# Optimization experiments

Measured on AMD Instinct MI355X. Metric: run time of the kernel, lower is better.

## Reference

```python
import jax, jax.numpy as jnp
import numpy as np

N, D, C = 2048, 192, 100000
S, M = 30.0, 0.2

def setup_inputs() -> dict:
    key = jax.random.key(0)
    k1, k2, k3 = jax.random.split(key, 3)
    x = jax.random.normal(k1, (N, D), dtype=jnp.float32)
    W = jax.random.normal(k2, (C, D), dtype=jnp.float32) * 0.05
    label = jax.random.randint(k3, (N,), 0, C, dtype=jnp.int64)
    return {"x": x, "W": W, "label": label}

def reference(x, W, label):
    # NOTE: the original torch code's weight-normalization loop is a no-op
    # (it rebinds the local name W, never mutating the parameter), so W is
    # intentionally NOT normalized here; only x is.
    xn = x / jnp.linalg.norm(x, axis=1, keepdims=True)          # [N, D]
    wf = jnp.einsum("nd,cd->nc", xn, W)                          # [N, C]
    tgt = jnp.take_along_axis(wf, label[:, None], axis=1)[:, 0]  # [N]
    numer = S * (tgt - M)                                        # margin-adjusted target logit
    logits = S * wf
    # replace the label column with the margin-adjusted numerator so that
    # logsumexp(logits) == log(exp(numer) + sum_{j!=y} exp(s*wf[:,j]))
    logits = logits.at[jnp.arange(N), label].set(numer)
    L = numer - jax.nn.logsumexp(logits, axis=1)                 # [N]
    return -jnp.mean(L)
```

## Files before the change

kernel.cpp:

```cpp
#include <hip/hip_runtime.h>
#include <stdint.h>


constexpr int N  = 2048;
constexpr int D  = 192;
constexpr int C  = 100000;
constexpr int KT = D / 32;
constexpr int TILE = 512;
constexpr int RT16 = C / 16;
constexpr int TPG = 12;
constexpr int CX = 523;
constexpr int NT16 = CX * TPG;
constexpr float PHANTOM = (float)(NT16 * 16 - C);
constexpr int BANDS = 4;
constexpr int RYB = N / (64 * BANDS);
constexpr int BUF = 4 * KT * TILE;
constexpr int NXB = N / 4;

#define S_SCALE 30.0f
#define MARGIN  0.2f
#define S_LOG2E 43.2808512266689f

using short8 = __attribute__((ext_vector_type(8))) short;
using f32x4  = __attribute__((ext_vector_type(4))) float;

typedef __attribute__((address_space(1))) const void GV;
typedef __attribute__((address_space(3))) void LV;

__device__ inline unsigned short f2bf(float f) {
  unsigned int u = __float_as_uint(f);
  u += 0x7fffu + ((u >> 16) & 1u);
  return (unsigned short)(u >> 16);
}

__device__ inline int pack_idx(int r, int k) {
  return ((r >> 4) * KT + (k >> 5)) * TILE + (((k >> 3) & 3) * 16 + (r & 15)) * 8 + (k & 7);
}

__device__ inline float row_sum16(float v) {
  int x;
  x = __float_as_int(v);
  v += __int_as_float(__builtin_amdgcn_update_dpp(0, x, 0x128, 0xF, 0xF, true));
  x = __float_as_int(v);
  v += __int_as_float(__builtin_amdgcn_update_dpp(0, x, 0x124, 0xF, 0xF, true));
  x = __float_as_int(v);
  v += __int_as_float(__builtin_amdgcn_update_dpp(0, x, 0x04E, 0xF, 0xF, true));
  x = __float_as_int(v);
  v += __int_as_float(__builtin_amdgcn_update_dpp(0, x, 0x0B1, 0xF, 0xF, true));
  return v;
}

__global__ __launch_bounds__(256) void prep_x(
    const float* __restrict__ x, unsigned short* __restrict__ xnb,
    float* __restrict__ out) {
  const int bid  = blockIdx.x;
  const int lane = threadIdx.x & 63;
  if (bid == 0 && threadIdx.x == 0) out[0] = 0.0f;

  const int row = bid * 4 + (threadIdx.x >> 6);
  const float* xr = x + (size_t)row * D;
  float v0 = xr[lane], v1 = xr[lane + 64], v2 = xr[lane + 128];
  float ss = v0 * v0 + v1 * v1 + v2 * v2;
#pragma unroll
  for (int off = 32; off > 0; off >>= 1) ss += __shfl_xor(ss, off, 64);
  const float inv = rsqrtf(ss) * S_LOG2E;
  xnb[pack_idx(row, lane)]       = f2bf(v0 * inv);
  xnb[pack_idx(row, lane + 64)]  = f2bf(v1 * inv);
  xnb[pack_idx(row, lane + 128)] = f2bf(v2 * inv);
}

__global__ __launch_bounds__(256, 3) void gemm_lse(
    const unsigned short* __restrict__ xnb,
    const float* __restrict__ W,
    float* __restrict__ partial) {
  __shared__ alignas(16) unsigned short As[2 * BUF];
  __shared__ alignas(16) float rs_lds[4][256];

  const int tid = threadIdx.x;
  const int bid = blockIdx.x;
  const int cx = bid >> 3, ry = bid & 7;

  {
    const unsigned short* slab = xnb + (size_t)(ry * BANDS) * BUF;
#pragma unroll
    for (int i = 0; i < 6; ++i) {
      const int chunk = tid + i * 256;
      __builtin_amdgcn_global_load_lds(
          (GV*)((const char*)slab + (size_t)chunk * 16),
          (LV*)((char*)As + (size_t)chunk * 16), 16, 0, 0);
    }
  }

  const int lane = tid & 63, wave = tid >> 6;
  const int m = lane & 15, quad = lane >> 4;

  short8 breg[3][KT];
#pragma unroll
  for (int tc = 0; tc < 3; ++tc) {
    const int t16 = cx * TPG + wave * 3 + tc;
    if (t16 < RT16) {
      const float* src = W + (size_t)(t16 * 16 + m) * D + quad * 8;
#pragma unroll
      for (int ks = 0; ks < KT; ++ks) {
        const float4* s4 = (const float4*)(src + ks * 32);
        float4 f0 = s4[0], f1 = s4[1];
        short8 hv;
        hv[0] = (short)f2bf(f0.x); hv[1] = (short)f2bf(f0.y);
        hv[2] = (short)f2bf(f0.z); hv[3] = (short)f2bf(f0.w);
        hv[4] = (short)f2bf(f1.x); hv[5] = (short)f2bf(f1.y);
        hv[6] = (short)f2bf(f1.z); hv[7] = (short)f2bf(f1.w);
        breg[tc][ks] = hv;
      }
    } else {
      const short8 z = {0, 0, 0, 0, 0, 0, 0, 0};
#pragma unroll
      for (int ks = 0; ks < KT; ++ks) breg[tc][ks] = z;
    }
  }

  const f32x4 zero4 = {0.0f, 0.0f, 0.0f, 0.0f};

  for (int b = 0; b < BANDS; ++b) {
    __syncthreads();

    if (b + 1 < BANDS) {
      const unsigned short* slab = xnb + (size_t)(ry * BANDS + b + 1) * BUF;
      char* dst = (char*)&As[((b + 1) & 1) * BUF];
#pragma unroll
      for (int i = 0; i < 6; ++i) {
        const int chunk = tid + i * 256;
        __builtin_amdgcn_global_load_lds(
            (GV*)((const char*)slab + (size_t)chunk * 16),
            (LV*)(dst + (size_t)chunk * 16), 16, 0, 0);
      }
    }

    const unsigned short* Ab = &As[(b & 1) * BUF];

    f32x4 acc[4][3];
#pragma unroll
    for (int a = 0; a < 4; ++a)
#pragma unroll
      for (int c = 0; c < 3; ++c) acc[a][c] = zero4;

#pragma unroll
    for (int ks = 0; ks < KT; ++ks) {
      short8 af[4];
#pragma unroll
      for (int tr = 0; tr < 4; ++tr)
        af[tr] = *(const short8*)(&Ab[(tr * KT + ks) * TILE + lane * 8]);
#pragma unroll
      for (int tr = 0; tr < 4; ++tr)
#pragma unroll
        for (int tc = 0; tc < 3; ++tc)
          acc[tr][tc] = __builtin_amdgcn_mfma_f32_16x16x32_bf16(
              af[tr], breg[tc][ks], acc[tr][tc], 0, 0, 0);
    }

#pragma unroll
    for (int tr = 0; tr < 4; ++tr) {
      float rv0 = 0.f, rv1 = 0.f, rv2 = 0.f, rv3 = 0.f;
#pragma unroll
      for (int tc = 0; tc < 3; ++tc) {
        rv0 += __builtin_amdgcn_exp2f(acc[tr][tc][0]);
        rv1 += __builtin_amdgcn_exp2f(acc[tr][tc][1]);
        rv2 += __builtin_amdgcn_exp2f(acc[tr][tc][2]);
        rv3 += __builtin_amdgcn_exp2f(acc[tr][tc][3]);
      }
      rv0 = row_sum16(rv0);
      rv1 = row_sum16(rv1);
      rv2 = row_sum16(rv2);
      rv3 = row_sum16(rv3);
      if (m == 0) {
        float4 v = make_float4(rv0, rv1, rv2, rv3);
        *(float4*)(&rs_lds[wave][b * 64 + tr * 16 + quad * 4]) = v;
      }
    }
  }

  __syncthreads();
  if (tid < 256) {
    const float s = rs_lds[0][tid] + rs_lds[1][tid] + rs_lds[2][tid] + rs_lds[3][tid];
    partial[(size_t)cx * N + ry * 256 + tid] = s;
  }
}

__global__ __launch_bounds__(256) void finalize_rows(
    const float* __restrict__ x, const float* __restrict__ W,
    const int* __restrict__ label, const float* __restrict__ partial,
    float* __restrict__ out) {
  const int row  = blockIdx.x * 4 + (threadIdx.x >> 6);
  const int lane = threadIdx.x & 63;
  const float* xr = x + (size_t)row * D;
  float v0 = xr[lane], v1 = xr[lane + 64], v2 = xr[lane + 128];
  float ss = v0 * v0 + v1 * v1 + v2 * v2;
  const int lab = label[row];
  const float* wr = W + (size_t)lab * D;
  float d = v0 * wr[lane] + v1 * wr[lane + 64] + v2 * wr[lane + 128];
  float p = 0.0f;
  for (int s = lane; s < CX; s += 64) p += partial[(size_t)s * N + row];
#pragma unroll
  for (int off = 32; off > 0; off >>= 1) {
    ss += __shfl_xor(ss, off, 64);
    d  += __shfl_xor(d,  off, 64);
    p  += __shfl_xor(p,  off, 64);
  }
  __shared__ float part[4];
  if (lane == 0) {
    const float tgt   = d * rsqrtf(ss);
    const float numer = S_SCALE * (tgt - MARGIN);
    const float se = p - PHANTOM - __expf(S_SCALE * tgt) + __expf(numer);
    part[threadIdx.x >> 6] = numer - logf(se);
  }
  __syncthreads();
  if (threadIdx.x == 0) {
    const float blocksum = part[0] + part[1] + part[2] + part[3];
    atomicAdd(out, -blocksum * (1.0f / (float)N));
  }
}

extern "C" void kernel_launch(void* const* d_in, const int* in_sizes, int n_in,
                              void* d_out, int out_size, void* d_ws, size_t ws_size,
                              hipStream_t stream) {
  const float* x     = (const float*)d_in[0];
  const float* W     = (const float*)d_in[1];
  const int*   label = (const int*)d_in[2];
  float*       out   = (float*)d_out;

  char* ws = (char*)d_ws;
  size_t off = 0;
  unsigned short* xnb = (unsigned short*)(ws + off); off += (size_t)N * D * 2;
  float* partial = (float*)(ws + off); off += (size_t)CX * N * 4;

  prep_x<<<NXB, 256, 0, stream>>>(x, xnb, out);

  gemm_lse<<<CX * RYB, 256, 0, stream>>>(xnb, W, partial);

  finalize_rows<<<N / 4, 256, 0, stream>>>(x, W, label, partial, out);
}
```

Measured before the change: 216.2 us.

## Make gemm_lse persistent with XCD-aware work assignment and cross-tile x prefetch

Replaces the one-block-per-tile grid with a persistent grid of 768 blocks. Each block loops over (column tile, row quarter) work items, with column tiles assigned per XCD, and doubles the bands per item so each converted W register tile is reused across more rows. It prefetches the first x band of the next work item during the last band, streams per-band row sums out with double-buffered LDS instead of a single end-of-item write, and converts W to bf16 with the packed v_cvt_pk_bf16_f32 instruction. The aim is to cut launch and tail overhead and to lower W reload and conversion cost, in exchange for more complex loop control and fewer resident blocks.

```diff
diff --git a/kernel.cpp b/kernel.cpp
--- a/kernel.cpp
+++ b/kernel.cpp
@@ -12,10 +12,14 @@
 constexpr int CX = 523;
 constexpr int NT16 = CX * TPG;
 constexpr float PHANTOM = (float)(NT16 * 16 - C);
-constexpr int BANDS = 4;
+constexpr int BANDS = 8;
 constexpr int RYB = N / (64 * BANDS);
 constexpr int BUF = 4 * KT * TILE;
 constexpr int NXB = N / 4;
+constexpr int CXG = 66;
+constexpr int JMAX = CXG * RYB;
+constexpr int SLOTS = 96;
+constexpr int GRID = SLOTS * 8;
 
 #define S_SCALE 30.0f
 #define MARGIN  0.2f
@@ -31,6 +35,12 @@
   unsigned int u = __float_as_uint(f);
   u += 0x7fffu + ((u >> 16) & 1u);
   return (unsigned short)(u >> 16);
+}
+
+__device__ inline unsigned int cvtpk(float lo, float hi) {
+  unsigned int r;
+  asm("v_cvt_pk_bf16_f32 %0, %1, %2" : "=v"(r) : "v"(lo), "v"(hi));
+  return r;
 }
 
 __device__ inline int pack_idx(int r, int k) {
@@ -69,119 +79,131 @@
   xnb[pack_idx(row, lane + 128)] = f2bf(v2 * inv);
 }
 
+#define DMA_BAND(DSTBYTES, SLABIDX)                                          \
+  {                                                                          \
+    const char* _src = (const char*)(xnb + (size_t)(SLABIDX) * BUF);         \
+    char* _dst = (char*)As + (size_t)(DSTBYTES);                             \
+    _Pragma("unroll")                                                        \
+    for (int _i = 0; _i < 6; ++_i) {                                         \
+      const int _c = tid + _i * 256;                                         \
+      __builtin_amdgcn_global_load_lds((GV*)(_src + (size_t)_c * 16),        \
+                                       (LV*)(_dst + (size_t)_c * 16), 16, 0, 0); \
+    }                                                                        \
+  }
+
 __global__ __launch_bounds__(256, 3) void gemm_lse(
     const unsigned short* __restrict__ xnb,
     const float* __restrict__ W,
     float* __restrict__ partial) {
   __shared__ alignas(16) unsigned short As[2 * BUF];
-  __shared__ alignas(16) float rs_lds[4][256];
+  __shared__ alignas(16) float rs[2][4][64];
 
   const int tid = threadIdx.x;
   const int bid = blockIdx.x;
-  const int cx = bid >> 3, ry = bid & 7;
-
-  {
-    const unsigned short* slab = xnb + (size_t)(ry * BANDS) * BUF;
-#pragma unroll
-    for (int i = 0; i < 6; ++i) {
-      const int chunk = tid + i * 256;
-      __builtin_amdgcn_global_load_lds(
-          (GV*)((const char*)slab + (size_t)chunk * 16),
-          (LV*)((char*)As + (size_t)chunk * 16), 16, 0, 0);
-    }
-  }
-
+  const int xcd = bid & 7, slot = bid >> 3;
   const int lane = tid & 63, wave = tid >> 6;
   const int m = lane & 15, quad = lane >> 4;
 
-  short8 breg[3][KT];
-#pragma unroll
-  for (int tc = 0; tc < 3; ++tc) {
-    const int t16 = cx * TPG + wave * 3 + tc;
-    if (t16 < RT16) {
-      const float* src = W + (size_t)(t16 * 16 + m) * D + quad * 8;
+  DMA_BAND(0, (slot & 3) * BANDS);
+
+  for (int j = slot; j < JMAX; j += SLOTS) {
+    const int ry = j & 3;
+    const int cx = (j >> 2) * 8 + xcd;
+    if (cx >= CX) break;
+    const int jn = j + SLOTS;
+    const bool next_ok = (jn < JMAX) && (((jn >> 2) * 8 + xcd) < CX);
+    const int ryn = jn & 3;
+
+    short8 breg[3][KT];
+#pragma unroll
+    for (int tc = 0; tc < 3; ++tc) {
+      const int t16 = cx * TPG + wave * 3 + tc;
+      if (t16 < RT16) {
+        const float* src = W + (size_t)(t16 * 16 + m) * D + quad * 8;
+#pragma unroll
+        for (int ks = 0; ks < KT; ++ks) {
+          const float4* s4 = (const float4*)(src + ks * 32);
+          float4 f0 = s4[0], f1 = s4[1];
+          union { uint4 u; short8 s; } cv;
+          cv.u.x = cvtpk(f0.x, f0.y);
+          cv.u.y = cvtpk(f0.z, f0.w);
+          cv.u.z = cvtpk(f1.x, f1.y);
+          cv.u.w = cvtpk(f1.z, f1.w);
+          breg[tc][ks] = cv.s;
+        }
+      } else {
+        const short8 z = {0, 0, 0, 0, 0, 0, 0, 0};
+#pragma unroll
+        for (int ks = 0; ks < KT; ++ks) breg[tc][ks] = z;
+      }
+    }
+
+    const f32x4 zero4 = {0.0f, 0.0f, 0.0f, 0.0f};
+
+    for (int b = 0; b < BANDS; ++b) {
+      __syncthreads();
+
+      if (b + 1 < BANDS) {
+        DMA_BAND(((b + 1) & 1) * (BUF * 2), ry * BANDS + b + 1);
+      } else if (next_ok) {
+        DMA_BAND(0, ryn * BANDS);
+      }
+
+      if (b >= 1 && tid < 64) {
+        const int pb = (b - 1) & 1;
+        const float s = rs[pb][0][tid] + rs[pb][1][tid] +
+                        rs[pb][2][tid] + rs[pb][3][tid];
+        partial[(size_t)cx * N + ry * (BANDS * 64) + (b - 1) * 64 + tid] = s;
+      }
+
+      const unsigned short* Ab = &As[(b & 1) * BUF];
+
+      f32x4 acc[4][3];
+#pragma unroll
+      for (int a = 0; a < 4; ++a)
+#pragma unroll
+        for (int c = 0; c < 3; ++c) acc[a][c] = zero4;
+
 #pragma unroll
       for (int ks = 0; ks < KT; ++ks) {
-        const float4* s4 = (const float4*)(src + ks * 32);
-        float4 f0 = s4[0], f1 = s4[1];
-        short8 hv;
-        hv[0] = (short)f2bf(f0.x); hv[1] = (short)f2bf(f0.y);
-        hv[2] = (short)f2bf(f0.z); hv[3] = (short)f2bf(f0.w);
-        hv[4] = (short)f2bf(f1.x); hv[5] = (short)f2bf(f1.y);
-        hv[6] = (short)f2bf(f1.z); hv[7] = (short)f2bf(f1.w);
-        breg[tc][ks] = hv;
-      }
-    } else {
-      const short8 z = {0, 0, 0, 0, 0, 0, 0, 0};
-#pragma unroll
-      for (int ks = 0; ks < KT; ++ks) breg[tc][ks] = z;
+        short8 af[4];
+#pragma unroll
+        for (int tr = 0; tr < 4; ++tr)
+          af[tr] = *(const short8*)(&Ab[(tr * KT + ks) * TILE + lane * 8]);
+#pragma unroll
+        for (int tr = 0; tr < 4; ++tr)
+#pragma unroll
+          for (int tc = 0; tc < 3; ++tc)
+            acc[tr][tc] = __builtin_amdgcn_mfma_f32_16x16x32_bf16(
+                af[tr], breg[tc][ks], acc[tr][tc], 0, 0, 0);
+      }
+
+#pragma unroll
+      for (int tr = 0; tr < 4; ++tr) {
+        float rv0 = 0.f, rv1 = 0.f, rv2 = 0.f, rv3 = 0.f;
+#pragma unroll
+        for (int tc = 0; tc < 3; ++tc) {
+          rv0 += __builtin_amdgcn_exp2f(acc[tr][tc][0]);
+          rv1 += __builtin_amdgcn_exp2f(acc[tr][tc][1]);
+          rv2 += __builtin_amdgcn_exp2f(acc[tr][tc][2]);
+          rv3 += __builtin_amdgcn_exp2f(acc[tr][tc][3]);
+        }
+        rv0 = row_sum16(rv0);
+        rv1 = row_sum16(rv1);
+        rv2 = row_sum16(rv2);
+        rv3 = row_sum16(rv3);
+        if (m == 0) {
+          float4 v = make_float4(rv0, rv1, rv2, rv3);
+          *(float4*)(&rs[b & 1][wave][tr * 16 + quad * 4]) = v;
+        }
+      }
     }
-  }
-
-  const f32x4 zero4 = {0.0f, 0.0f, 0.0f, 0.0f};
-
-  for (int b = 0; b < BANDS; ++b) {
+
     __syncthreads();
-
-    if (b + 1 < BANDS) {
-      const unsigned short* slab = xnb + (size_t)(ry * BANDS + b + 1) * BUF;
-      char* dst = (char*)&As[((b + 1) & 1) * BUF];
-#pragma unroll
-      for (int i = 0; i < 6; ++i) {
-        const int chunk = tid + i * 256;
-        __builtin_amdgcn_global_load_lds(
-            (GV*)((const char*)slab + (size_t)chunk * 16),
-            (LV*)(dst + (size_t)chunk * 16), 16, 0, 0);
-      }
+    if (tid < 64) {
+      const float s = rs[1][0][tid] + rs[1][1][tid] + rs[1][2][tid] + rs[1][3][tid];
+      partial[(size_t)cx * N + ry * (BANDS * 64) + (BANDS - 1) * 64 + tid] = s;
     }
-
-    const unsigned short* Ab = &As[(b & 1) * BUF];
-
-    f32x4 acc[4][3];
-#pragma unroll
-    for (int a = 0; a < 4; ++a)
-#pragma unroll
-      for (int c = 0; c < 3; ++c) acc[a][c] = zero4;
-
-#pragma unroll
-    for (int ks = 0; ks < KT; ++ks) {
-      short8 af[4];
-#pragma unroll
-      for (int tr = 0; tr < 4; ++tr)
-        af[tr] = *(const short8*)(&Ab[(tr * KT + ks) * TILE + lane * 8]);
-#pragma unroll
-      for (int tr = 0; tr < 4; ++tr)
-#pragma unroll
-        for (int tc = 0; tc < 3; ++tc)
-          acc[tr][tc] = __builtin_amdgcn_mfma_f32_16x16x32_bf16(
-              af[tr], breg[tc][ks], acc[tr][tc], 0, 0, 0);
-    }
-
-#pragma unroll
-    for (int tr = 0; tr < 4; ++tr) {
-      float rv0 = 0.f, rv1 = 0.f, rv2 = 0.f, rv3 = 0.f;
-#pragma unroll
-      for (int tc = 0; tc < 3; ++tc) {
-        rv0 += __builtin_amdgcn_exp2f(acc[tr][tc][0]);
-        rv1 += __builtin_amdgcn_exp2f(acc[tr][tc][1]);
-        rv2 += __builtin_amdgcn_exp2f(acc[tr][tc][2]);
-        rv3 += __builtin_amdgcn_exp2f(acc[tr][tc][3]);
-      }
-      rv0 = row_sum16(rv0);
-      rv1 = row_sum16(rv1);
-      rv2 = row_sum16(rv2);
-      rv3 = row_sum16(rv3);
-      if (m == 0) {
-        float4 v = make_float4(rv0, rv1, rv2, rv3);
-        *(float4*)(&rs_lds[wave][b * 64 + tr * 16 + quad * 4]) = v;
-      }
-    }
-  }
-
-  __syncthreads();
-  if (tid < 256) {
-    const float s = rs_lds[0][tid] + rs_lds[1][tid] + rs_lds[2][tid] + rs_lds[3][tid];
-    partial[(size_t)cx * N + ry * 256 + tid] = s;
   }
 }
 
@@ -234,7 +256,7 @@
 
   prep_x<<<NXB, 256, 0, stream>>>(x, xnb, out);
 
-  gemm_lse<<<CX * RYB, 256, 0, stream>>>(xnb, W, partial);
+  gemm_lse<<<GRID, 256, 0, stream>>>(xnb, W, partial);
 
   finalize_rows<<<N / 4, 256, 0, stream>>>(x, W, label, partial, out);
 }
```

Result: slower. 220.8 us (+2.1%).
